# Performance work log

Measured on AMD Instinct MI355X. Metric: run time of the kernel, lower is better.

The kernel has to match this reference:

```python
import jax, jax.numpy as jnp
import numpy as np

N = 100000      # num vertices
NE = 20000      # num hyperedges
NNZ = 1600000   # incidence pairs
NFEAT = 128
NHID = 64       # nhid * nhead = 8 * 8
NCLASS = 40
NLAYER = 4
ALPHA = 0.1
LAMDA = 0.5


def setup_inputs() -> dict:
    key = jax.random.key(0)
    ks = jax.random.split(key, 9)
    x = jax.random.normal(ks[0], (N, NFEAT), dtype=jnp.float32)
    vertex = jax.random.randint(ks[1], (NNZ,), 0, N, dtype=jnp.int32)
    edges = jax.random.randint(ks[2], (NNZ,), 0, NE, dtype=jnp.int32)
    degE = jax.random.uniform(ks[3], (NE, 1), dtype=jnp.float32)
    degV = jax.random.uniform(ks[4], (N, 1), dtype=jnp.float32)
    W0 = jax.random.normal(ks[5], (NFEAT, NHID), dtype=jnp.float32) * 0.05
    b0 = jnp.zeros((NHID,), jnp.float32)
    Ws = jax.random.normal(ks[6], (NLAYER, NHID, NHID), dtype=jnp.float32) * 0.05
    Wout = jax.random.normal(ks[7], (NHID, NCLASS), dtype=jnp.float32) * 0.05
    bout = jnp.zeros((NCLASS,), jnp.float32)
    return dict(x=x, degE=degE, degV=degV, W0=W0, b0=b0, Ws=Ws,
                Wout=Wout, bout=bout, vertex=vertex, edges=edges)


def _normalize_l2(X):
    # torch: norm computed on detached X, inf scales zeroed
    norm = jnp.linalg.norm(jax.lax.stop_gradient(X), axis=1, keepdims=True)
    scale = jnp.where(norm > 0, 1.0 / norm, 0.0)
    return X * scale


def reference(x, degE, degV, W0, b0, Ws, Wout, bout, vertex, edges):
    # per-hyperedge member counts for the 'mean' first_aggregate
    counts = jax.ops.segment_sum(jnp.ones((NNZ,), x.dtype), edges, num_segments=NE)
    counts = jnp.maximum(counts, 1.0)[:, None]  # [NE,1]

    X = jax.nn.relu(x @ W0 + b0)   # [N, NHID]
    X0 = X
    for i in range(NLAYER):
        beta = float(np.log(LAMDA / (i + 1) + 1.0))
        Xve = X[vertex]                                                   # [NNZ, NHID]
        Xe = jax.ops.segment_sum(Xve, edges, num_segments=NE) / counts   # vertex->edge mean
        Xe = Xe * degE                                                    # [NE, NHID]
        Xev = Xe[edges]                                                   # [NNZ, NHID]
        Xv = jax.ops.segment_sum(Xev, vertex, num_segments=N) * degV     # edge->vertex sum
        Xn = _normalize_l2(Xv)                                            # use_norm=True
        Xi = (1.0 - ALPHA) * Xn + ALPHA * X0
        X = jax.nn.relu((1.0 - beta) * Xi + beta * (Xi @ Ws[i]))
    logits = X @ Wout + bout
    return jax.nn.log_softmax(logits, axis=1)
```

## Files before the change

kernel.cpp:

```cpp
#include <hip/hip_runtime.h>
#include <math.h>

constexpr int NV   = 100000;
constexpr int NEg  = 20000;
constexpr int NNZp = 1600000;
constexpr int NF   = 128;
constexpr int NH   = 64;
constexpr int NC   = 40;

constexpr int WE  = 64;
constexpr int NBE = (NEg + WE - 1) / WE;
constexpr int WV  = 256;
constexpr int NBV = (NV + WV - 1) / WV;
constexpr int SB  = NBE + NBV;
constexpr int CAPS = 6400;
constexpr int CH   = 4096;
constexpr int PBLK = (NNZp + CH - 1) / CH;

typedef __bf16 bf16x8 __attribute__((ext_vector_type(8)));
typedef float  f32x4  __attribute__((ext_vector_type(4)));
typedef unsigned short u16x8 __attribute__((ext_vector_type(8)));

__device__ __forceinline__ float bf2f(unsigned short u) {
    unsigned int x = ((unsigned int)u) << 16;
    return __builtin_bit_cast(float, x);
}
__device__ __forceinline__ unsigned short f2bf(float f) {
    unsigned int x = __builtin_bit_cast(unsigned int, f);
    x += 0x7fffu + ((x >> 16) & 1u);
    return (unsigned short)(x >> 16);
}
__device__ __forceinline__ ushort4 pack4(float a, float b, float c, float d) {
    ushort4 u; u.x = f2bf(a); u.y = f2bf(b); u.z = f2bf(c); u.w = f2bf(d);
    return u;
}
__device__ __forceinline__ void acc8(float* a, u16x8 p) {
#pragma unroll
    for (int k = 0; k < 8; ++k) a[k] += bf2f(p[k]);
}

__device__ __forceinline__ int block_excl_scan(int val, int tid, int* wtot) {
    __syncthreads();
    int x = val;
#pragma unroll
    for (int o = 1; o < 64; o <<= 1) {
        int y = __shfl_up(x, o);
        if ((tid & 63) >= o) x += y;
    }
    if ((tid & 63) == 63) wtot[tid >> 6] = x;
    __syncthreads();
    int add = 0;
    const int w = tid >> 6;
#pragma unroll
    for (int k = 0; k < 7; ++k) add += (k < w) ? wtot[k] : 0;
    return add + x - val;
}

__global__ __launch_bounds__(256) void coarse_hist(const int* __restrict__ vertex,
                                                   const int* __restrict__ edges,
                                                   int* __restrict__ cnt_be,
                                                   int* __restrict__ cnt_bv,
                                                   int* __restrict__ bhist) {
    __shared__ int he[NBE], hv[NBV];
    for (int i = threadIdx.x; i < NBE; i += 256) he[i] = 0;
    for (int i = threadIdx.x; i < NBV; i += 256) hv[i] = 0;
    __syncthreads();
    const int base = blockIdx.x * CH;
    const int end  = min(base + CH, NNZp);
    for (int i = base + threadIdx.x; i < end; i += 256) {
        atomicAdd(&he[edges[i]  >> 6], 1);
        atomicAdd(&hv[vertex[i] >> 8], 1);
    }
    __syncthreads();
    int* row = bhist + (size_t)blockIdx.x * SB;
    for (int i = threadIdx.x; i < NBE; i += 256) {
        int h = he[i];
        row[i] = h;
        if (h) atomicAdd(&cnt_be[i], h);
    }
    for (int i = threadIdx.x; i < NBV; i += 256) {
        int h = hv[i];
        row[NBE + i] = h;
        if (h) atomicAdd(&cnt_bv[i], h);
    }
}

__global__ __launch_bounds__(512) void scan_buckets(const int* __restrict__ cnt_be,
                                                    const int* __restrict__ cnt_bv,
                                                    int* __restrict__ rsb_e,
                                                    int* __restrict__ rsb_v,
                                                    int* __restrict__ rs_e,
                                                    int* __restrict__ rs_v) {
    __shared__ int s[512];
    const int n      = (blockIdx.x == 0) ? NBE : NBV;
    const int* c     = (blockIdx.x == 0) ? cnt_be : cnt_bv;
    int* r           = (blockIdx.x == 0) ? rsb_e : rsb_v;
    const int t = threadIdx.x;
    int v = (t < n) ? c[t] : 0;
    s[t] = v;
    __syncthreads();
    for (int o = 1; o < 512; o <<= 1) {
        int u = (t >= o) ? s[t - o] : 0;
        __syncthreads();
        s[t] += u;
        __syncthreads();
    }
    if (t < n) r[t] = s[t] - v;
    if (t == 0) {
        r[n] = NNZp;
        if (blockIdx.x == 0) rs_e[NEg] = NNZp;
        else                 rs_v[NV]  = NNZp;
    }
}

__global__ __launch_bounds__(512) void colscan(const int* __restrict__ bhist,
                                               const int* __restrict__ rsb_e,
                                               const int* __restrict__ rsb_v,
                                               int* __restrict__ abase) {
    __shared__ int s[512];
    const int f = blockIdx.x;
    const int t = threadIdx.x;
    int v = (t < PBLK) ? bhist[(size_t)t * SB + f] : 0;
    s[t] = v;
    __syncthreads();
    for (int o = 1; o < 512; o <<= 1) {
        int u = (t >= o) ? s[t - o] : 0;
        __syncthreads();
        s[t] += u;
        __syncthreads();
    }
    const int base = (f < NBE) ? rsb_e[f] : rsb_v[f - NBE];
    if (t < PBLK) abase[(size_t)t * SB + f] = base + (s[t] - v);
}

__global__ __launch_bounds__(512) void partition_both(const int* __restrict__ vertex,
                                                      const int* __restrict__ edges,
                                                      const int* __restrict__ bhist,
                                                      const int* __restrict__ abase,
                                                      int* __restrict__ vid_out,
                                                      int* __restrict__ eid_out) {
    __shared__ int sval_e[CH], sdst_e[CH];
    __shared__ int sval_v[CH], sdst_v[CH];
    __shared__ int off_e[NBE], gb_e[NBE], cnt_e[NBE];
    __shared__ int off_v[NBV], gb_v[NBV], cnt_v[NBV];
    __shared__ int wtot[8];
    const int tid = threadIdx.x;
    const int b = blockIdx.x;
    const int* bh = bhist + (size_t)b * SB;
    const int* ab = abase + (size_t)b * SB;
    for (int i = tid; i < NBE; i += 512) { cnt_e[i] = 0; gb_e[i] = ab[i]; }
    for (int i = tid; i < NBV; i += 512) { cnt_v[i] = 0; gb_v[i] = ab[NBE + i]; }
    {
        int h  = (tid < NBE) ? bh[tid] : 0;
        int ex = block_excl_scan(h, tid, wtot);
        if (tid < NBE) off_e[tid] = ex;
    }
    {
        int h  = (tid < NBV) ? bh[NBE + tid] : 0;
        int ex = block_excl_scan(h, tid, wtot);
        if (tid < NBV) off_v[tid] = ex;
    }
    __syncthreads();
    const int base = b * CH;
    const int n    = min(base + CH, NNZp) - base;
    for (int i = tid; i < n; i += 512) {
        int e = edges[base + i];
        int v = vertex[base + i];
        int fe = e >> 6;
        int rk = atomicAdd(&cnt_e[fe], 1);
        int sl = off_e[fe] + rk;
        sval_e[sl] = (v << 6) | (e & 63);
        sdst_e[sl] = gb_e[fe] + rk;
        int fv = v >> 8;
        int rv = atomicAdd(&cnt_v[fv], 1);
        int s2 = off_v[fv] + rv;
        sval_v[s2] = (e << 8) | (v & 255);
        sdst_v[s2] = gb_v[fv] + rv;
    }
    __syncthreads();
    for (int i = tid; i < n; i += 512) {
        vid_out[sdst_e[i]] = sval_e[i];
        eid_out[sdst_v[i]] = sval_v[i];
    }
}

__global__ __launch_bounds__(512) void local_sort_both(const int* __restrict__ rsb_e,
                                                       const int* __restrict__ rsb_v,
                                                       int* __restrict__ vid_buf,
                                                       int* __restrict__ eid_buf,
                                                       int* __restrict__ rs_e,
                                                       int* __restrict__ rs_v,
                                                       const float* __restrict__ degE,
                                                       float* __restrict__ scaleE) {
    __shared__ int stage[CAPS];
    __shared__ int hist[256], off[256], cnt2[256];
    const bool eside = blockIdx.x < NBE;
    const int b   = eside ? blockIdx.x : blockIdx.x - NBE;
    const int W   = eside ? 64 : 256;
    const int FB  = eside ? 6 : 8;
    const int NID = eside ? NEg : NV;
    const int* rsb = eside ? rsb_e : rsb_v;
    int* buf       = eside ? vid_buf : eid_buf;
    int* rs        = eside ? rs_e : rs_v;
    const int base = rsb[b];
    const int sz   = rsb[b + 1] - base;
    const int tid = threadIdx.x;
    if (tid < 256) { hist[tid] = 0; cnt2[tid] = 0; }
    __syncthreads();
    for (int t = tid; t < sz; t += 512) atomicAdd(&hist[buf[base + t] & (W - 1)], 1);
    __syncthreads();
    {
        int v = (tid < W) ? hist[tid] : 0;
        if (tid < W) off[tid] = v;
        __syncthreads();
        for (int o = 1; o < W; o <<= 1) {
            int u = (tid < W && tid >= o) ? off[tid - o] : 0;
            __syncthreads();
            if (tid < W) off[tid] += u;
            __syncthreads();
        }
        if (tid < W) off[tid] -= v;
    }
    if (tid < W) {
        int gid = b * W + tid;
        if (gid < NID) {
            rs[gid] = base + off[tid];
            if (eside) {
                int c = hist[tid];
                scaleE[gid] = degE[gid] / (float)(c < 1 ? 1 : c);
            }
        }
    }
    __syncthreads();
    for (int t = tid; t < sz; t += 512) {
        int w = buf[base + t];
        int f = w & (W - 1);
        int rk = off[f] + atomicAdd(&cnt2[f], 1);
        stage[rk] = w >> FB;
    }
    __syncthreads();
    for (int t = tid; t < sz; t += 512) buf[base + t] = stage[t];
}

__global__ __launch_bounds__(256) void make_wfrag(const float* __restrict__ Ws,
                                                  const float* __restrict__ Wout,
                                                  const float* __restrict__ W0,
                                                  unsigned short* __restrict__ frag) {
    int t = blockIdx.x * 256 + threadIdx.x;
    int lane = t & 63;
    int g = t >> 6;
    int quad = lane >> 4, cl = lane & 15;
    unsigned short o[8];
    if (g < 32) {
        int li = g >> 3, w = (g >> 1) & 3, kh = g & 1;
        int n = w * 16 + cl;
#pragma unroll
        for (int j = 0; j < 8; ++j) {
            int k = kh * 32 + quad * 8 + j;
            o[j] = f2bf(Ws[(size_t)li * NH * NH + k * NH + n]);
        }
    } else if (g < 40) {
        int w = (g - 32) >> 1, kh = g & 1;
        int n = w * 16 + cl;
#pragma unroll
        for (int j = 0; j < 8; ++j) {
            int k = kh * 32 + quad * 8 + j;
            o[j] = (n < NC) ? f2bf(Wout[k * NC + n]) : (unsigned short)0;
        }
    } else {
        int w = (g - 40) >> 2, kb = (g - 40) & 3;
        int n = w * 16 + cl;
#pragma unroll
        for (int j = 0; j < 8; ++j) {
            int k = kb * 32 + quad * 8 + j;
            o[j] = f2bf(W0[k * NH + n]);
        }
    }
    unsigned short* dst = frag + (size_t)g * 512 + lane * 8;
    *((ushort4*)dst)       = *(ushort4*)&o[0];
    *((ushort4*)(dst + 4)) = *(ushort4*)&o[4];
}

__global__ __launch_bounds__(256) void gemm0_kernel(const float* __restrict__ x,
                                                    const unsigned short* __restrict__ W0frag,
                                                    const float* __restrict__ b0,
                                                    unsigned short* __restrict__ Xbf,
                                                    unsigned short* __restrict__ X0bf) {
    __shared__ unsigned short xs[16][136];
    const int tid = threadIdx.x;
    const int r  = tid >> 4;
    const int c8 = (tid & 15) * 8;
    const int rowbase = blockIdx.x * 16;
    float4 p0 = *((const float4*)(x + (size_t)(rowbase + r) * NF + c8));
    float4 p1 = *((const float4*)(x + (size_t)(rowbase + r) * NF + c8 + 4));
    *((ushort4*)&xs[r][c8])     = pack4(p0.x, p0.y, p0.z, p0.w);
    *((ushort4*)&xs[r][c8 + 4]) = pack4(p1.x, p1.y, p1.z, p1.w);
    __syncthreads();
    const int lane = tid & 63;
    const int wv   = tid >> 6;
    const int quad = lane >> 4;
    const int cl   = lane & 15;
    f32x4 acc = {0.f, 0.f, 0.f, 0.f};
#pragma unroll
    for (int kb = 0; kb < 4; ++kb) {
        bf16x8 a = *((const bf16x8*)&xs[cl][kb * 32 + quad * 8]);
        bf16x8 b = *((const bf16x8*)(W0frag + ((size_t)(wv * 4 + kb) * 64 + lane) * 8));
        acc = __builtin_amdgcn_mfma_f32_16x16x32_bf16(a, b, acc, 0, 0, 0);
    }
    const int col = wv * 16 + cl;
    const float bo = b0[col];
#pragma unroll
    for (int p = 0; p < 4; ++p) {
        const int orow = quad * 4 + p;
        float o = acc[p] + bo;
        o = o > 0.f ? o : 0.f;
        unsigned short ob = f2bf(o);
        const size_t idx = (size_t)(rowbase + orow) * NH + col;
        Xbf[idx]  = ob;
        X0bf[idx] = ob;
    }
}

__global__ __launch_bounds__(256) void gather_ve(const int* __restrict__ rs_e,
                                                 const int* __restrict__ vid_sorted,
                                                 const unsigned short* __restrict__ Xbf,
                                                 const float* __restrict__ scaleE,
                                                 unsigned short* __restrict__ Xebf) {
    const int tid = threadIdx.x;
    const int l8  = tid & 7;
    const int e = blockIdx.x * 16 + (tid >> 4);
    const int sb = rs_e[e];
    const int se = rs_e[e + 1];
    const int h  = (se - sb + 1) >> 1;
    int m        = sb + ((tid & 8) ? h : 0);
    const int en = (tid & 8) ? se : (sb + h);
    float a[8] = {0.f, 0.f, 0.f, 0.f, 0.f, 0.f, 0.f, 0.f};
    const int nfull = (en - m) >> 3;
    if (nfull >= 2) {
        int idB[8];
        u16x8 dA[8];
        {
            int idA[8];
#pragma unroll
            for (int j = 0; j < 8; ++j) idA[j] = vid_sorted[m + j];
#pragma unroll
            for (int j = 0; j < 8; ++j)
                dA[j] = *((const u16x8*)(Xbf + (size_t)idA[j] * NH) + l8);
        }
#pragma unroll
        for (int j = 0; j < 8; ++j) idB[j] = vid_sorted[m + 8 + j];
        m += 16;
        for (int c = 2; c < nfull; ++c) {
            u16x8 dB[8];
#pragma unroll
            for (int j = 0; j < 8; ++j)
                dB[j] = *((const u16x8*)(Xbf + (size_t)idB[j] * NH) + l8);
#pragma unroll
            for (int j = 0; j < 8; ++j) idB[j] = vid_sorted[m + j];
            m += 8;
#pragma unroll
            for (int j = 0; j < 8; ++j) acc8(a, dA[j]);
#pragma unroll
            for (int j = 0; j < 8; ++j) dA[j] = dB[j];
        }
        {
            u16x8 dB[8];
#pragma unroll
            for (int j = 0; j < 8; ++j)
                dB[j] = *((const u16x8*)(Xbf + (size_t)idB[j] * NH) + l8);
#pragma unroll
            for (int j = 0; j < 8; ++j) acc8(a, dA[j]);
#pragma unroll
            for (int j = 0; j < 8; ++j) acc8(a, dB[j]);
        }
    } else if (nfull == 1) {
        int id[8];
        u16x8 d[8];
#pragma unroll
        for (int j = 0; j < 8; ++j) id[j] = vid_sorted[m + j];
#pragma unroll
        for (int j = 0; j < 8; ++j)
            d[j] = *((const u16x8*)(Xbf + (size_t)id[j] * NH) + l8);
        m += 8;
#pragma unroll
        for (int j = 0; j < 8; ++j) acc8(a, d[j]);
    }
    for (; m < en; ++m) {
        u16x8 p = *((const u16x8*)(Xbf + (size_t)vid_sorted[m] * NH) + l8);
        acc8(a, p);
    }
#pragma unroll
    for (int j = 0; j < 8; ++j) a[j] += __shfl_xor(a[j], 8);
    if (!(tid & 8)) {
        const float s = scaleE[e];
        u16x8 o;
#pragma unroll
        for (int j = 0; j < 8; ++j) o[j] = f2bf(a[j] * s);
        *((u16x8*)(Xebf + (size_t)e * NH) + l8) = o;
    }
}

template <bool LAST>
__global__ __launch_bounds__(256) void gather_ev_update(const int* __restrict__ rs_v,
                                                        const int* __restrict__ eid_sorted,
                                                        const unsigned short* __restrict__ Xebf,
                                                        const float* __restrict__ degV,
                                                        const unsigned short* __restrict__ X0bf,
                                                        const unsigned short* __restrict__ WfragL,
                                                        unsigned short* __restrict__ Xbf,
                                                        float beta,
                                                        const unsigned short* __restrict__ WfragH,
                                                        const float* __restrict__ bout,
                                                        float* __restrict__ outp) {
    __shared__ unsigned short xis_bf[16][72];
    __shared__ unsigned short xo_bf[LAST ? 16 * 72 : 1];
    __shared__ float lg[LAST ? 16 * 48 : 1];
    const int tid = threadIdx.x;
    const int l8  = tid & 7;
    const int r   = tid >> 4;
    const int v = blockIdx.x * 16 + r;
    const int sb  = rs_v[v];
    const int sen = rs_v[v + 1];
    const float dv = degV[v];
    const int h  = (sen - sb + 1) >> 1;
    int m        = sb + ((tid & 8) ? h : 0);
    const int en = (tid & 8) ? sen : (sb + h);
    float a[8] = {0.f, 0.f, 0.f, 0.f, 0.f, 0.f, 0.f, 0.f};
    const int nfull = (en - m) >> 2;
    if (nfull >= 2) {
        int idB[4];
        u16x8 dA[4];
        {
            int idA[4];
#pragma unroll
            for (int j = 0; j < 4; ++j) idA[j] = eid_sorted[m + j];
#pragma unroll
            for (int j = 0; j < 4; ++j)
                dA[j] = *((const u16x8*)(Xebf + (size_t)idA[j] * NH) + l8);
        }
#pragma unroll
        for (int j = 0; j < 4; ++j) idB[j] = eid_sorted[m + 4 + j];
        m += 8;
        for (int c = 2; c < nfull; ++c) {
            u16x8 dB[4];
#pragma unroll
            for (int j = 0; j < 4; ++j)
                dB[j] = *((const u16x8*)(Xebf + (size_t)idB[j] * NH) + l8);
#pragma unroll
            for (int j = 0; j < 4; ++j) idB[j] = eid_sorted[m + j];
            m += 4;
#pragma unroll
            for (int j = 0; j < 4; ++j) acc8(a, dA[j]);
#pragma unroll
            for (int j = 0; j < 4; ++j) dA[j] = dB[j];
        }
        {
            u16x8 dB[4];
#pragma unroll
            for (int j = 0; j < 4; ++j)
                dB[j] = *((const u16x8*)(Xebf + (size_t)idB[j] * NH) + l8);
#pragma unroll
            for (int j = 0; j < 4; ++j) acc8(a, dA[j]);
#pragma unroll
            for (int j = 0; j < 4; ++j) acc8(a, dB[j]);
        }
    } else if (nfull == 1) {
        int id[4];
        u16x8 d[4];
#pragma unroll
        for (int j = 0; j < 4; ++j) id[j] = eid_sorted[m + j];
#pragma unroll
        for (int j = 0; j < 4; ++j)
            d[j] = *((const u16x8*)(Xebf + (size_t)id[j] * NH) + l8);
        m += 4;
#pragma unroll
        for (int j = 0; j < 4; ++j) acc8(a, d[j]);
    }
    for (; m < en; ++m) {
        u16x8 p = *((const u16x8*)(Xebf + (size_t)eid_sorted[m] * NH) + l8);
        acc8(a, p);
    }
#pragma unroll
    for (int j = 0; j < 8; ++j) {
        a[j] += __shfl_xor(a[j], 8);
        a[j] *= dv;
    }
    float sq = 0.f;
#pragma unroll
    for (int j = 0; j < 8; ++j) sq += a[j] * a[j];
    sq += __shfl_xor(sq, 1);
    sq += __shfl_xor(sq, 2);
    sq += __shfl_xor(sq, 4);
    float norm = sqrtf(sq);
    float inv = norm > 0.f ? 1.f / norm : 0.f;
    u16x8 u0 = *((const u16x8*)(X0bf + (size_t)v * NH) + l8);
    if (!(tid & 8)) {
        u16x8 o;
#pragma unroll
        for (int j = 0; j < 8; ++j) o[j] = f2bf(0.9f * a[j] * inv + 0.1f * bf2f(u0[j]));
        *((u16x8*)&xis_bf[r][l8 * 8]) = o;
    }
    __syncthreads();

    const int lane = tid & 63;
    const int wv   = tid >> 6;
    const int quad = lane >> 4;
    const int cl   = lane & 15;
    bf16x8 bw0 = *((const bf16x8*)(WfragL + ((size_t)(wv * 2 + 0) * 64 + lane) * 8));
    bf16x8 bw1 = *((const bf16x8*)(WfragL + ((size_t)(wv * 2 + 1) * 64 + lane) * 8));
    bf16x8 a0 = *((const bf16x8*)&xis_bf[cl][quad * 8]);
    bf16x8 a1 = *((const bf16x8*)&xis_bf[cl][32 + quad * 8]);
    f32x4 acc = {0.f, 0.f, 0.f, 0.f};
    acc = __builtin_amdgcn_mfma_f32_16x16x32_bf16(a0, bw0, acc, 0, 0, 0);
    acc = __builtin_amdgcn_mfma_f32_16x16x32_bf16(a1, bw1, acc, 0, 0, 0);

    const float ob = 1.f - beta;
    const int col = wv * 16 + cl;
#pragma unroll
    for (int p = 0; p < 4; ++p) {
        const int row = quad * 4 + p;
        float xiv = bf2f(xis_bf[row][col]);
        float o = ob * xiv + beta * acc[p];
        o = o > 0.f ? o : 0.f;
        if (!LAST) {
            Xbf[(size_t)(blockIdx.x * 16 + row) * NH + col] = f2bf(o);
        } else {
            xo_bf[row * 72 + col] = f2bf(o);
        }
    }
    if (LAST) {
        __syncthreads();
        bf16x8 bh0 = *((const bf16x8*)(WfragH + ((size_t)(wv * 2 + 0) * 64 + lane) * 8));
        bf16x8 bh1 = *((const bf16x8*)(WfragH + ((size_t)(wv * 2 + 1) * 64 + lane) * 8));
        bf16x8 ah0 = *((const bf16x8*)&xo_bf[cl * 72 + quad * 8]);
        bf16x8 ah1 = *((const bf16x8*)&xo_bf[cl * 72 + 32 + quad * 8]);
        f32x4 acch = {0.f, 0.f, 0.f, 0.f};
        acch = __builtin_amdgcn_mfma_f32_16x16x32_bf16(ah0, bh0, acch, 0, 0, 0);
        acch = __builtin_amdgcn_mfma_f32_16x16x32_bf16(ah1, bh1, acch, 0, 0, 0);
        if (col < NC) {
            float bo = bout[col];
#pragma unroll
            for (int p = 0; p < 4; ++p) lg[(quad * 4 + p) * 48 + col] = acch[p] + bo;
        }
        __syncthreads();
        const int r0 = wv * 4;
        const bool act = lane < NC;
        float a0s = act ? lg[(r0 + 0) * 48 + lane] : -INFINITY;
        float a1s = act ? lg[(r0 + 1) * 48 + lane] : -INFINITY;
        float a2s = act ? lg[(r0 + 2) * 48 + lane] : -INFINITY;
        float a3s = act ? lg[(r0 + 3) * 48 + lane] : -INFINITY;
        float m0 = a0s, m1 = a1s, m2 = a2s, m3 = a3s;
#pragma unroll
        for (int o = 32; o; o >>= 1) {
            m0 = fmaxf(m0, __shfl_xor(m0, o));
            m1 = fmaxf(m1, __shfl_xor(m1, o));
            m2 = fmaxf(m2, __shfl_xor(m2, o));
            m3 = fmaxf(m3, __shfl_xor(m3, o));
        }
        float e0 = act ? expf(a0s - m0) : 0.f;
        float e1 = act ? expf(a1s - m1) : 0.f;
        float e2 = act ? expf(a2s - m2) : 0.f;
        float e3 = act ? expf(a3s - m3) : 0.f;
#pragma unroll
        for (int o = 32; o; o >>= 1) {
            e0 += __shfl_xor(e0, o);
            e1 += __shfl_xor(e1, o);
            e2 += __shfl_xor(e2, o);
            e3 += __shfl_xor(e3, o);
        }
        if (act) {
            const size_t vb = (size_t)(blockIdx.x * 16 + r0) * NC + lane;
            outp[vb + 0 * NC] = a0s - m0 - logf(e0);
            outp[vb + 1 * NC] = a1s - m1 - logf(e1);
            outp[vb + 2 * NC] = a2s - m2 - logf(e2);
            outp[vb + 3 * NC] = a3s - m3 - logf(e3);
        }
    }
}

extern "C" void kernel_launch(void* const* d_in, const int* in_sizes, int n_in,
                              void* d_out, int out_size, void* d_ws, size_t ws_size,
                              hipStream_t stream) {
    const float* x    = (const float*)d_in[0];
    const float* degE = (const float*)d_in[1];
    const float* degV = (const float*)d_in[2];
    const float* W0   = (const float*)d_in[3];
    const float* b0   = (const float*)d_in[4];
    const float* Ws   = (const float*)d_in[5];
    const float* Wout = (const float*)d_in[6];
    const float* bout = (const float*)d_in[7];
    const int* vertex = (const int*)d_in[8];
    const int* edges  = (const int*)d_in[9];
    float* out = (float*)d_out;

    float* scaleE = (float*)d_ws;
    unsigned short* Xbf  = (unsigned short*)(scaleE + NEg);
    unsigned short* X0bf = Xbf + (size_t)NV * NH;
    unsigned short* Xebf = X0bf + (size_t)NV * NH;
    int* cnt_be = (int*)(Xebf + (size_t)NEg * NH);
    int* cnt_bv = cnt_be + NBE;
    int* rsb_e  = cnt_bv + NBV;
    int* rsb_v  = rsb_e + (NBE + 1);
    int* rs_e   = rsb_v + (NBV + 1);
    int* rs_v   = rs_e + (NEg + 1);
    int* vid_sorted = rs_v + (NV + 1);
    int* eid_sorted = vid_sorted + NNZp;
    unsigned short* Wfrag = (unsigned short*)(eid_sorted + NNZp);
    int* bhist = (int*)(Wfrag + 56 * 512);
    int* abase = bhist + (size_t)PBLK * SB;

    hipMemsetAsync(cnt_be, 0, (size_t)(NBE + NBV) * sizeof(int), stream);
    make_wfrag<<<14, 256, 0, stream>>>(Ws, Wout, W0, Wfrag);
    coarse_hist<<<PBLK, 256, 0, stream>>>(vertex, edges, cnt_be, cnt_bv, bhist);
    scan_buckets<<<2, 512, 0, stream>>>(cnt_be, cnt_bv, rsb_e, rsb_v, rs_e, rs_v);
    colscan<<<SB, 512, 0, stream>>>(bhist, rsb_e, rsb_v, abase);
    partition_both<<<PBLK, 512, 0, stream>>>(vertex, edges, bhist, abase,
                                             vid_sorted, eid_sorted);
    local_sort_both<<<NBE + NBV, 512, 0, stream>>>(rsb_e, rsb_v, vid_sorted, eid_sorted,
                                                   rs_e, rs_v, degE, scaleE);

    gemm0_kernel<<<NV / 16, 256, 0, stream>>>(x, Wfrag + 40 * 512, b0, Xbf, X0bf);

    const float betas[4] = {logf(0.5f / 1.f + 1.f), logf(0.5f / 2.f + 1.f),
                            logf(0.5f / 3.f + 1.f), logf(0.5f / 4.f + 1.f)};

    for (int i = 0; i < 3; ++i) {
        gather_ve<<<NEg / 16, 256, 0, stream>>>(rs_e, vid_sorted, Xbf, scaleE, Xebf);
        gather_ev_update<false><<<NV / 16, 256, 0, stream>>>(rs_v, eid_sorted, Xebf, degV,
                                                             X0bf, Wfrag + (size_t)i * 4096,
                                                             Xbf, betas[i],
                                                             nullptr, nullptr, nullptr);
    }
    gather_ve<<<NEg / 16, 256, 0, stream>>>(rs_e, vid_sorted, Xbf, scaleE, Xebf);
    gather_ev_update<true><<<NV / 16, 256, 0, stream>>>(rs_v, eid_sorted, Xebf, degV,
                                                        X0bf, Wfrag + (size_t)3 * 4096,
                                                        Xbf, betas[3],
                                                        Wfrag + 16384, bout, out);
}
```

Before: 425.2 us.

## Store hyperedge features in fp32, pre-scale sorted indices, simplify gather pipelining

The intermediate hyperedge feature buffer moves from bf16 to fp32. This removes bf16 pack/unpack work in both gather kernels, at the cost of twice the gathered bytes per edge row in the edge-to-vertex phase. The local sort now stores row offsets (index << 6) instead of raw indices, which removes the multiply in every gathered address. Both gather loops are rewritten from an 8-deep/4-deep double-buffered prefetch into a simpler 4-wide index-prefetch loop, which may reduce memory-level parallelism in the vertex-to-edge gather.

After: 421.7 us. No clear change (-0.8%).

```diff
diff --git a/kernel.cpp b/kernel.cpp
--- a/kernel.cpp
+++ b/kernel.cpp
@@ -37,6 +37,10 @@
 __device__ __forceinline__ void acc8(float* a, u16x8 p) {
 #pragma unroll
     for (int k = 0; k < 8; ++k) a[k] += bf2f(p[k]);
+}
+__device__ __forceinline__ void accf(float* a, float4 p, float4 q) {
+    a[0] += p.x; a[1] += p.y; a[2] += p.z; a[3] += p.w;
+    a[4] += q.x; a[5] += q.y; a[6] += q.z; a[7] += q.w;
 }
 
 __device__ __forceinline__ int block_excl_scan(int val, int tid, int* wtot) {
@@ -236,7 +240,7 @@
         int w = buf[base + t];
         int f = w & (W - 1);
         int rk = off[f] + atomicAdd(&cnt2[f], 1);
-        stage[rk] = w >> FB;
+        stage[rk] = (w >> FB) << 6;
     }
     __syncthreads();
     for (int t = tid; t < sz; t += 512) buf[base + t] = stage[t];
@@ -325,7 +329,7 @@
                                                  const int* __restrict__ vid_sorted,
                                                  const unsigned short* __restrict__ Xbf,
                                                  const float* __restrict__ scaleE,
-                                                 unsigned short* __restrict__ Xebf) {
+                                                 float* __restrict__ Xef) {
     const int tid = threadIdx.x;
     const int l8  = tid & 7;
     const int e = blockIdx.x * 16 + (tid >> 4);
@@ -335,75 +339,48 @@
     int m        = sb + ((tid & 8) ? h : 0);
     const int en = (tid & 8) ? se : (sb + h);
     float a[8] = {0.f, 0.f, 0.f, 0.f, 0.f, 0.f, 0.f, 0.f};
-    const int nfull = (en - m) >> 3;
-    if (nfull >= 2) {
-        int idB[8];
-        u16x8 dA[8];
-        {
-            int idA[8];
-#pragma unroll
-            for (int j = 0; j < 8; ++j) idA[j] = vid_sorted[m + j];
-#pragma unroll
-            for (int j = 0; j < 8; ++j)
-                dA[j] = *((const u16x8*)(Xbf + (size_t)idA[j] * NH) + l8);
-        }
-#pragma unroll
-        for (int j = 0; j < 8; ++j) idB[j] = vid_sorted[m + 8 + j];
-        m += 16;
-        for (int c = 2; c < nfull; ++c) {
-            u16x8 dB[8];
-#pragma unroll
-            for (int j = 0; j < 8; ++j)
-                dB[j] = *((const u16x8*)(Xbf + (size_t)idB[j] * NH) + l8);
-#pragma unroll
-            for (int j = 0; j < 8; ++j) idB[j] = vid_sorted[m + j];
-            m += 8;
-#pragma unroll
-            for (int j = 0; j < 8; ++j) acc8(a, dA[j]);
-#pragma unroll
-            for (int j = 0; j < 8; ++j) dA[j] = dB[j];
-        }
-        {
-            u16x8 dB[8];
-#pragma unroll
-            for (int j = 0; j < 8; ++j)
-                dB[j] = *((const u16x8*)(Xbf + (size_t)idB[j] * NH) + l8);
-#pragma unroll
-            for (int j = 0; j < 8; ++j) acc8(a, dA[j]);
-#pragma unroll
-            for (int j = 0; j < 8; ++j) acc8(a, dB[j]);
-        }
-    } else if (nfull == 1) {
-        int id[8];
-        u16x8 d[8];
-#pragma unroll
-        for (int j = 0; j < 8; ++j) id[j] = vid_sorted[m + j];
-#pragma unroll
-        for (int j = 0; j < 8; ++j)
-            d[j] = *((const u16x8*)(Xbf + (size_t)id[j] * NH) + l8);
-        m += 8;
-#pragma unroll
-        for (int j = 0; j < 8; ++j) acc8(a, d[j]);
+    if (m + 4 <= en) {
+        int i0 = vid_sorted[m], i1 = vid_sorted[m + 1];
+        int i2 = vid_sorted[m + 2], i3 = vid_sorted[m + 3];
+        m += 4;
+        while (m + 4 <= en) {
+            int j0 = vid_sorted[m], j1 = vid_sorted[m + 1];
+            int j2 = vid_sorted[m + 2], j3 = vid_sorted[m + 3];
+            m += 4;
+            u16x8 p = *((const u16x8*)(Xbf + i0) + l8);
+            u16x8 q = *((const u16x8*)(Xbf + i1) + l8);
+            u16x8 u = *((const u16x8*)(Xbf + i2) + l8);
+            u16x8 t = *((const u16x8*)(Xbf + i3) + l8);
+            acc8(a, p); acc8(a, q); acc8(a, u); acc8(a, t);
+            i0 = j0; i1 = j1; i2 = j2; i3 = j3;
+        }
+        u16x8 p = *((const u16x8*)(Xbf + i0) + l8);
+        u16x8 q = *((const u16x8*)(Xbf + i1) + l8);
+        u16x8 u = *((const u16x8*)(Xbf + i2) + l8);
+        u16x8 t = *((const u16x8*)(Xbf + i3) + l8);
+        acc8(a, p); acc8(a, q); acc8(a, u); acc8(a, t);
     }
     for (; m < en; ++m) {
-        u16x8 p = *((const u16x8*)(Xbf + (size_t)vid_sorted[m] * NH) + l8);
+        u16x8 p = *((const u16x8*)(Xbf + vid_sorted[m]) + l8);
         acc8(a, p);
     }
 #pragma unroll
     for (int j = 0; j < 8; ++j) a[j] += __shfl_xor(a[j], 8);
     if (!(tid & 8)) {
         const float s = scaleE[e];
-        u16x8 o;
-#pragma unroll
-        for (int j = 0; j < 8; ++j) o[j] = f2bf(a[j] * s);
-        *((u16x8*)(Xebf + (size_t)e * NH) + l8) = o;
+        float4 o0, o1;
+        o0.x = a[0] * s; o0.y = a[1] * s; o0.z = a[2] * s; o0.w = a[3] * s;
+        o1.x = a[4] * s; o1.y = a[5] * s; o1.z = a[6] * s; o1.w = a[7] * s;
+        float* dst = Xef + e * NH + l8 * 8;
+        *((float4*)dst)       = o0;
+        *((float4*)(dst + 4)) = o1;
     }
 }
 
 template <bool LAST>
 __global__ __launch_bounds__(256) void gather_ev_update(const int* __restrict__ rs_v,
                                                         const int* __restrict__ eid_sorted,
-                                                        const unsigned short* __restrict__ Xebf,
+                                                        const float* __restrict__ Xef,
                                                         const float* __restrict__ degV,
                                                         const unsigned short* __restrict__ X0bf,
                                                         const unsigned short* __restrict__ WfragL,
@@ -426,59 +403,39 @@
     int m        = sb + ((tid & 8) ? h : 0);
     const int en = (tid & 8) ? sen : (sb + h);
     float a[8] = {0.f, 0.f, 0.f, 0.f, 0.f, 0.f, 0.f, 0.f};
-    const int nfull = (en - m) >> 2;
-    if (nfull >= 2) {
-        int idB[4];
-        u16x8 dA[4];
-        {
-            int idA[4];
-#pragma unroll
-            for (int j = 0; j < 4; ++j) idA[j] = eid_sorted[m + j];
-#pragma unroll
-            for (int j = 0; j < 4; ++j)
-                dA[j] = *((const u16x8*)(Xebf + (size_t)idA[j] * NH) + l8);
-        }
-#pragma unroll
-        for (int j = 0; j < 4; ++j) idB[j] = eid_sorted[m + 4 + j];
-        m += 8;
-        for (int c = 2; c < nfull; ++c) {
-            u16x8 dB[4];
-#pragma unroll
-            for (int j = 0; j < 4; ++j)
-                dB[j] = *((const u16x8*)(Xebf + (size_t)idB[j] * NH) + l8);
-#pragma unroll
-            for (int j = 0; j < 4; ++j) idB[j] = eid_sorted[m + j];
+    if (m + 4 <= en) {
+        int i0 = eid_sorted[m], i1 = eid_sorted[m + 1];
+        int i2 = eid_sorted[m + 2], i3 = eid_sorted[m + 3];
+        m += 4;
+        while (m + 4 <= en) {
+            int j0 = eid_sorted[m], j1 = eid_sorted[m + 1];
+            int j2 = eid_sorted[m + 2], j3 = eid_sorted[m + 3];
             m += 4;
-#pragma unroll
-            for (int j = 0; j < 4; ++j) acc8(a, dA[j]);
-#pragma unroll
-            for (int j = 0; j < 4; ++j) dA[j] = dB[j];
-        }
-        {
-            u16x8 dB[4];
-#pragma unroll
-            for (int j = 0; j < 4; ++j)
-                dB[j] = *((const u16x8*)(Xebf + (size_t)idB[j] * NH) + l8);
-#pragma unroll
-            for (int j = 0; j < 4; ++j) acc8(a, dA[j]);
-#pragma unroll
-            for (int j = 0; j < 4; ++j) acc8(a, dB[j]);
-        }
-    } else if (nfull == 1) {
-        int id[4];
-        u16x8 d[4];
-#pragma unroll
-        for (int j = 0; j < 4; ++j) id[j] = eid_sorted[m + j];
-#pragma unroll
-        for (int j = 0; j < 4; ++j)
-            d[j] = *((const u16x8*)(Xebf + (size_t)id[j] * NH) + l8);
-        m += 4;
-#pragma unroll
-        for (int j = 0; j < 4; ++j) acc8(a, d[j]);
+            const float4* r0 = (const float4*)(Xef + i0) + (l8 << 1);
+            const float4* r1 = (const float4*)(Xef + i1) + (l8 << 1);
+            const float4* r2 = (const float4*)(Xef + i2) + (l8 << 1);
+            const float4* r3 = (const float4*)(Xef + i3) + (l8 << 1);
+            float4 p0 = r0[0], p1 = r0[1];
+            float4 q0 = r1[0], q1 = r1[1];
+            float4 u0 = r2[0], u1 = r2[1];
+            float4 t0 = r3[0], t1 = r3[1];
+            accf(a, p0, p1); accf(a, q0, q1); accf(a, u0, u1); accf(a, t0, t1);
+            i0 = j0; i1 = j1; i2 = j2; i3 = j3;
+        }
+        const float4* r0 = (const float4*)(Xef + i0) + (l8 << 1);
+        const float4* r1 = (const float4*)(Xef + i1) + (l8 << 1);
+        const float4* r2 = (const float4*)(Xef + i2) + (l8 << 1);
+        const float4* r3 = (const float4*)(Xef + i3) + (l8 << 1);
+        float4 p0 = r0[0], p1 = r0[1];
+        float4 q0 = r1[0], q1 = r1[1];
+        float4 u0 = r2[0], u1 = r2[1];
+        float4 t0 = r3[0], t1 = r3[1];
+        accf(a, p0, p1); accf(a, q0, q1); accf(a, u0, u1); accf(a, t0, t1);
     }
     for (; m < en; ++m) {
-        u16x8 p = *((const u16x8*)(Xebf + (size_t)eid_sorted[m] * NH) + l8);
-        acc8(a, p);
+        const float4* rp = (const float4*)(Xef + eid_sorted[m]) + (l8 << 1);
+        float4 p0 = rp[0], p1 = rp[1];
+        accf(a, p0, p1);
     }
 #pragma unroll
     for (int j = 0; j < 8; ++j) {
@@ -493,11 +450,11 @@
     sq += __shfl_xor(sq, 4);
     float norm = sqrtf(sq);
     float inv = norm > 0.f ? 1.f / norm : 0.f;
-    u16x8 u0 = *((const u16x8*)(X0bf + (size_t)v * NH) + l8);
+    u16x8 x0 = *((const u16x8*)(X0bf + (size_t)v * NH) + l8);
     if (!(tid & 8)) {
         u16x8 o;
 #pragma unroll
-        for (int j = 0; j < 8; ++j) o[j] = f2bf(0.9f * a[j] * inv + 0.1f * bf2f(u0[j]));
+        for (int j = 0; j < 8; ++j) o[j] = f2bf(0.9f * a[j] * inv + 0.1f * bf2f(x0[j]));
         *((u16x8*)&xis_bf[r][l8 * 8]) = o;
     }
     __syncthreads();
@@ -596,8 +553,8 @@
     float* scaleE = (float*)d_ws;
     unsigned short* Xbf  = (unsigned short*)(scaleE + NEg);
     unsigned short* X0bf = Xbf + (size_t)NV * NH;
-    unsigned short* Xebf = X0bf + (size_t)NV * NH;
-    int* cnt_be = (int*)(Xebf + (size_t)NEg * NH);
+    float* Xef = (float*)(X0bf + (size_t)NV * NH);
+    int* cnt_be = (int*)(Xef + (size_t)NEg * NH);
     int* cnt_bv = cnt_be + NBE;
     int* rsb_e  = cnt_bv + NBV;
     int* rsb_v  = rsb_e + (NBE + 1);
@@ -625,14 +582,14 @@
                             logf(0.5f / 3.f + 1.f), logf(0.5f / 4.f + 1.f)};
 
     for (int i = 0; i < 3; ++i) {
-        gather_ve<<<NEg / 16, 256, 0, stream>>>(rs_e, vid_sorted, Xbf, scaleE, Xebf);
-        gather_ev_update<false><<<NV / 16, 256, 0, stream>>>(rs_v, eid_sorted, Xebf, degV,
+        gather_ve<<<NEg / 16, 256, 0, stream>>>(rs_e, vid_sorted, Xbf, scaleE, Xef);
+        gather_ev_update<false><<<NV / 16, 256, 0, stream>>>(rs_v, eid_sorted, Xef, degV,
                                                              X0bf, Wfrag + (size_t)i * 4096,
                                                              Xbf, betas[i],
                                                              nullptr, nullptr, nullptr);
     }
-    gather_ve<<<NEg / 16, 256, 0, stream>>>(rs_e, vid_sorted, Xbf, scaleE, Xebf);
-    gather_ev_update<true><<<NV / 16, 256, 0, stream>>>(rs_v, eid_sorted, Xebf, degV,
+    gather_ve<<<NEg / 16, 256, 0, stream>>>(rs_e, vid_sorted, Xbf, scaleE, Xef);
+    gather_ev_update<true><<<NV / 16, 256, 0, stream>>>(rs_v, eid_sorted, Xef, degV,
                                                         X0bf, Wfrag + (size_t)3 * 4096,
                                                         Xbf, betas[3],
                                                         Wfrag + 16384, bout, out);
```
